# Optimization experiments

Hardware: AMD Instinct MI355X
Metric: run time of the kernel (lower is better)

Reference implementation:

```python
import jax, jax.numpy as jnp
import numpy as np

B, N, F, H, D, HID = 32, 256, 8, 8, 8, 512  # batch, stocks, features, heads, head_dim, hidden
NEG_SLOPE = 0.2
NEG_INF = -1e30


def setup_inputs() -> dict:
    key = jax.random.key(0)
    ks = jax.random.split(key, 20)
    feat = jax.random.normal(ks[0], (B, F, N), jnp.float32)
    adjs = [(jax.random.uniform(ks[1 + i], (B, N, N)) < 0.05).astype(jnp.float32) for i in range(3)]
    inputs = jnp.concatenate(adjs + [feat], axis=1)  # (B, 3N+F, N)
    s = 0.02  # xavier-ish gain used in the torch init
    stdv = 1.0 / np.sqrt(H * D)
    return {
        'inputs': inputs,
        'W_gat': jax.random.normal(ks[4], (3, HID, H * D), jnp.float32) * stdv,
        'Wu': jax.random.normal(ks[5], (3, H, D, 1), jnp.float32),
        'Wv': jax.random.normal(ks[6], (3, H, D, 1), jnp.float32),
        'b_gat': jax.random.normal(ks[7], (3, H * D), jnp.float32) * stdv,
        'projW': jax.random.normal(ks[8], (3, HID, H * D), jnp.float32) * s,
        'projB': jnp.zeros((3, H * D), jnp.float32),
        'w_self1': jax.random.normal(ks[9], (F, HID), jnp.float32) * s,
        'b_self1': jnp.zeros((HID,), jnp.float32),
        'w_mlp': jax.random.normal(ks[10], (3, H * D, HID), jnp.float32) * s,
        'b_mlp': jnp.zeros((3, HID), jnp.float32),
        'w_self2': jax.random.normal(ks[11], (HID, HID), jnp.float32) * s,
        'b_self2': jnp.zeros((HID,), jnp.float32),
        'sem_w1': jax.random.normal(ks[12], (HID, HID), jnp.float32) * s,
        'sem_b1': jnp.zeros((HID,), jnp.float32),
        'sem_w2': jax.random.normal(ks[13], (HID, 1), jnp.float32) * s,
        'gen_w': jax.random.normal(ks[14], (N * HID, N), jnp.float32) * s,
        'gen_b': jnp.zeros((N,), jnp.float32),
    }


def _mhgat(x, adj, W, Wu, Wv, b, pW, pB):
    # x: (B,N,HID), adj: (B,N,N)
    # rows of adj that are entirely zero are replaced by 1e-6 everywhere
    adj = jnp.where(jnp.all(adj == 0, axis=-1, keepdims=True), 1e-6, adj)
    sup = (x @ W).reshape(B, N, H, D).transpose(0, 2, 1, 3)  # (B,H,N,D)
    f1 = jnp.einsum('bhnd,hd->bhn', sup, Wu[..., 0])[:, :, None, :]  # (B,H,1,N)
    f2 = jnp.einsum('bhnd,hd->bhn', sup, Wv[..., 0])[:, :, :, None]  # (B,H,N,1)
    w = jax.nn.leaky_relu(f1 + f2, NEG_SLOPE)  # (B,H,N,N)
    mw = jnp.einsum('bhij,bjk->bhik', w, adj)  # matmul masking, as in torch source
    mask = mw != 0
    # torch.sparse.softmax: softmax over nonzero entries only, zeros elsewhere
    attn = jax.nn.softmax(jnp.where(mask, mw, NEG_INF), axis=3)
    attn = jnp.where(mask, attn, 0.0)
    out = (attn @ sup).transpose(0, 2, 1, 3).reshape(B, N, H * D) + b
    out = out + x @ pW + pB  # residual projection
    return jnp.tanh(out)


def reference(inputs, W_gat, Wu, Wv, b_gat, projW, projB, w_self1, b_self1,
              w_mlp, b_mlp, w_self2, b_self2, sem_w1, sem_b1, sem_w2, gen_w, gen_b):
    ind_adj = inputs[:, :N, :]
    pos_adj = inputs[:, N:2 * N, :]
    neg_adj = inputs[:, 2 * N:3 * N, :]
    x = inputs[:, 3 * N:, :].transpose(0, 2, 1)  # (B,N,F)
    support = x @ w_self1 + b_self1  # (B,N,HID)
    gat_out = [_mhgat(support, a, W_gat[i], Wu[i], Wv[i], b_gat[i], projW[i], projB[i])
               for i, a in enumerate([ind_adj, pos_adj, neg_adj])]
    ind_s, pos_s, neg_s = gat_out
    s2 = support @ w_self2 + b_self2
    ind_o = ind_s @ w_mlp[0] + b_mlp[0]
    pos_o = neg_s @ w_mlp[1] + b_mlp[1]  # NOTE: bug in original source preserved (uses neg_support)
    neg_o = neg_s @ w_mlp[2] + b_mlp[2]
    emb = jnp.stack([s2, ind_o, pos_o, neg_o], axis=1)  # (B,4,N,HID)
    # semantic fusion attention
    wsem = jnp.tanh(emb @ sem_w1 + sem_b1) @ sem_w2  # (B,4,N,1)
    beta = jax.nn.softmax(wsem, axis=1)
    fused = (beta * emb).sum(axis=1)  # (B,N,HID)
    # PairNorm PN-SI, scale=1
    xc = fused - fused.mean(axis=1, keepdims=True)
    xc = xc / jnp.sqrt(1e-6 + (xc ** 2).sum(axis=2, keepdims=True))
    # generator
    flat = xc.reshape(B, N * HID)
    return jax.nn.sigmoid(flat @ gen_w + gen_b)  # (B,N)
```

## Files before the change

kernel.cpp:

```cpp
#include <hip/hip_runtime.h>
#include <math.h>

#define Bk   32
#define Nk   256
#define Fk   8
#define Hk   8
#define Dk   8
#define HIDk 512
#define HDk  64
#define NROWk 776
#define CAPk 96

typedef __attribute__((ext_vector_type(8))) short short8;
typedef __attribute__((ext_vector_type(4))) float f32x4;

__device__ __forceinline__ float lrelu(float x){ return fmaxf(x, 0.2f*x); }

__device__ __forceinline__ unsigned short f2bf(float x){
  unsigned int u = __float_as_uint(x);
  unsigned int r = (u + 0x7fffu + ((u>>16)&1u)) >> 16;
  return (unsigned short)r;
}

__global__ void k_support(const float* __restrict__ inp, const float* __restrict__ w1,
                          const float* __restrict__ b1, float* __restrict__ support){
  int bn = blockIdx.x; int b = bn >> 8; int n = bn & 255;
  const float* xin = inp + (size_t)b*NROWk*Nk + (size_t)(3*Nk)*Nk + n;
  float x[8];
#pragma unroll
  for (int f=0; f<8; f++) x[f] = xin[(size_t)f*Nk];
  int t = threadIdx.x;
  for (int c = t; c < HIDk; c += 256){
    float s = b1[c];
#pragma unroll
    for (int f=0; f<8; f++) s += x[f]*w1[f*HIDk + c];
    support[(size_t)bn*HIDk + c] = s;
  }
}

__global__ void k_sup(const float* __restrict__ support, const float* __restrict__ W,
                      float* __restrict__ sup){
  __shared__ float srow[4][HIDk+1];
  int b = blockIdx.x >> 6; int n0 = (blockIdx.x & 63) << 2;
  int t = threadIdx.x;
  for (int i = t; i < 4*HIDk; i += 256)
    srow[i>>9][i&511] = support[((size_t)b*Nk + n0 + (i>>9))*HIDk + (i&511)];
  __syncthreads();
  int nl = t >> 6, hd = t & 63;
  const float* srw = srow[nl];
  float s = 0.f;
  for (int c=0;c<HIDk;c++) s += srw[c]*W[c*HDk + hd];
  int h = hd >> 3, d = hd & 7;
  sup[(((size_t)b*Hk + h)*Nk + (n0+nl))*Dk + d] = s;
}

__global__ void k_fuv(const float* __restrict__ sup, const float* __restrict__ Wu,
                      const float* __restrict__ Wv, float* __restrict__ fu, float* __restrict__ fv){
  int i = blockIdx.x*256 + threadIdx.x;
  int h = (i >> 8) & 7;
  const float* s = sup + (size_t)i*Dk;
  float a=0.f, v=0.f;
#pragma unroll
  for (int d=0; d<8; d++){ float sv = s[d]; a += sv*Wu[h*8+d]; v += sv*Wv[h*8+d]; }
  fu[i] = a; fv[i] = v;
}

__global__ void k_rowzero(const float* __restrict__ inp, int rowOff,
                          int* __restrict__ z_cnt, int* __restrict__ z_idx){
  int b = blockIdx.x >> 8, j = blockIdx.x & 255;
  float v = inp[(size_t)b*NROWk*Nk + (size_t)(rowOff+j)*Nk + threadIdx.x];
  __shared__ int flag;
  if (threadIdx.x==0) flag = 0;
  __syncthreads();
  if (v != 0.0f) atomicOr(&flag, 1);
  __syncthreads();
  if (threadIdx.x==0 && flag==0){ int idx = atomicAdd(&z_cnt[b], 1); z_idx[b*Nk + idx] = j; }
}

__global__ void k_csc(const float* __restrict__ inp, int rowOff,
                      int* __restrict__ col_cnt, int* __restrict__ row_idx){
  int b = blockIdx.x >> 8, k = blockIdx.x & 255;
  int j = threadIdx.x;
  __shared__ unsigned char nzf[Nk];
  nzf[j] = (inp[(size_t)b*NROWk*Nk + (size_t)(rowOff+j)*Nk + k] != 0.0f) ? 1 : 0;
  __syncthreads();
  if (j == 0){
    int c = 0; int base = (b*Nk + k)*CAPk;
    for (int jj=0; jj<Nk; jj++) if (nzf[jj]){ if (c < CAPk) row_idx[base + c] = jj; c++; }
    col_cnt[b*Nk + k] = (c > CAPk) ? CAPk : c;
  }
}

__global__ void k_zsum(const float* __restrict__ fu, const float* __restrict__ fv,
                       const int* __restrict__ z_cnt, const int* __restrict__ z_idx,
                       float* __restrict__ zsum){
  int i = blockIdx.x*256 + threadIdx.x;
  int bh = i >> 8; int b = bh >> 3;
  int zc = z_cnt[b];
  float fvi = fv[i], s = 0.f;
  for (int t=0; t<zc; t++){ float x = fvi + fu[(bh<<8) + z_idx[b*Nk+t]]; s += lrelu(x); }
  zsum[i] = s;
}

__global__ __launch_bounds__(256) void k_attn(const float* __restrict__ sup,
    const float* __restrict__ fu_g, const float* __restrict__ fv_g,
    const float* __restrict__ zsum_g, const int* __restrict__ z_cnt,
    const int* __restrict__ col_cnt, const int* __restrict__ row_idx,
    float* __restrict__ ao){
  __shared__ float fu_s[Nk];
  __shared__ float fvt[32];
  __shared__ float zs[32];
  __shared__ float sup_s[Nk*Dk];
  __shared__ float mw[32][Nk+1];
  __shared__ unsigned char maskk[Nk];
  int blk = blockIdx.x;
  int bh = blk >> 3;
  int b  = bh >> 3;
  int h  = bh & 7;
  int i0 = (blk & 7) << 5;
  int t = threadIdx.x;
  fu_s[t] = fu_g[(bh<<8) + t];
  if (t < 32){ fvt[t] = fv_g[(bh<<8) + i0 + t]; zs[t] = zsum_g[(bh<<8) + i0 + t]; }
  for (int i = t; i < Nk*Dk; i += 256) sup_s[i] = sup[(size_t)bh*Nk*Dk + i];
  int zc = z_cnt[b];
  int cnt = col_cnt[b*Nk + t];
  maskk[t] = (cnt > 0 || zc > 0) ? 1 : 0;
  __syncthreads();
  {
    float acc[32];
#pragma unroll
    for (int i=0;i<32;i++) acc[i]=0.f;
    const int* ridx = row_idx + (size_t)(b*Nk + t)*CAPk;
    for (int s=0;s<cnt;s++){
      float fuj = fu_s[ridx[s]];
#pragma unroll
      for (int i=0;i<32;i++){ float x = fvt[i] + fuj; acc[i] += fmaxf(x, 0.2f*x); }
    }
#pragma unroll
    for (int i=0;i<32;i++) mw[i][t] = acc[i] + 1e-6f*zs[i];
  }
  __syncthreads();
  int wv = t>>6, lane = t&63;
  for (int i = wv; i < 32; i += 4){
    float vals[4]; float m = -1e30f;
#pragma unroll
    for (int q=0;q<4;q++){ int kk = lane + (q<<6); float v = mw[i][kk]; vals[q]=v; if (maskk[kk]) m = fmaxf(m, v); }
#pragma unroll
    for (int s=32;s>0;s>>=1) m = fmaxf(m, __shfl_xor(m, s));
    float e[4]; float sum=0.f;
#pragma unroll
    for (int q=0;q<4;q++){ int kk = lane + (q<<6); float p = maskk[kk] ? expf(vals[q]-m) : 0.f; e[q]=p; sum+=p; }
#pragma unroll
    for (int s=32;s>0;s>>=1) sum += __shfl_xor(sum, s);
    float inv = (sum > 0.f) ? 1.f/sum : 0.f;
#pragma unroll
    for (int q=0;q<4;q++){ int kk = lane + (q<<6); mw[i][kk] = e[q]*inv; }
  }
  __syncthreads();
  int il = t>>3, d = t&7;
  float s = 0.f;
  for (int kk=0; kk<Nk; kk++) s += mw[il][kk]*sup_s[kk*Dk + d];
  ao[((size_t)b*Nk + i0 + il)*HDk + (h<<3) + d] = s;
}

__global__ void k_gatout(const float* __restrict__ ao, const float* __restrict__ support,
                         const float* __restrict__ pW, const float* __restrict__ pB,
                         const float* __restrict__ bg, float* __restrict__ gat){
  __shared__ float srow[4][HIDk+1];
  int b = blockIdx.x >> 6; int n0 = (blockIdx.x & 63) << 2;
  int t = threadIdx.x;
  for (int i = t; i < 4*HIDk; i += 256)
    srow[i>>9][i&511] = support[((size_t)b*Nk + n0 + (i>>9))*HIDk + (i&511)];
  __syncthreads();
  int nl = t >> 6, hd = t & 63;
  const float* srw = srow[nl];
  float s = pB[hd] + bg[hd];
  for (int c=0;c<HIDk;c++) s += srw[c]*pW[c*HDk + hd];
  size_t idx = ((size_t)b*Nk + n0 + nl)*HDk + hd;
  gat[idx] = tanhf(s + ao[idx]);
}

__global__ void k_prepT(const float* __restrict__ w_self2, const float* __restrict__ sem_w1,
                        unsigned short* __restrict__ w2T, unsigned short* __restrict__ w1T){
  __shared__ float tile[64][65];
  const float* src = blockIdx.y ? sem_w1 : w_self2;
  unsigned short* dst = blockIdx.y ? w1T : w2T;
  int tk = (blockIdx.x >> 3) << 6;
  int tn = (blockIdx.x & 7) << 6;
  int t = threadIdx.x;
  for (int i = t; i < 64*64; i += 256){
    int r = i >> 6, c = i & 63;
    tile[r][c] = src[(size_t)(tk + r)*HIDk + tn + c];
  }
  __syncthreads();
  for (int i = t; i < 64*64; i += 256){
    int r = i >> 6, c = i & 63;
    dst[(size_t)(tn + r)*HIDk + tk + c] = f2bf(tile[c][r]);
  }
}

template<int MODE, int NF>
__global__ __launch_bounds__(256) void k_gemm512(
    const float* __restrict__ A, const unsigned short* __restrict__ BT,
    const float* __restrict__ bias, const float* __restrict__ w2,
    float* __restrict__ outf){
  constexpr int NPB = NF*16;
  __shared__ uint4 As4[64*4];
  __shared__ uint4 Bs4[NPB*4];
  int row0 = blockIdx.x << 6;
  int col0 = blockIdx.y * NPB;
  int t = threadIdx.x;
  int w = t >> 6, l = t & 63;
  f32x4 acc[NF];
#pragma unroll
  for (int i=0;i<NF;i++) acc[i] = (f32x4){0.f,0.f,0.f,0.f};

  int lrA = t >> 2;
  int slot = t & 3;
  const float* aptr = A + (size_t)(row0 + lrA)*HIDk + slot*8;
  const unsigned short* bbase = BT + (size_t)col0*HIDk + slot*8;

  for (int kc = 0; kc < 512; kc += 32){
    float4 av0 = *(const float4*)(aptr + kc);
    float4 av1 = *(const float4*)(aptr + kc + 4);
    uint4 bv[NPB/64];
#pragma unroll
    for (int r = 0; r < NPB/64; r++){
      int ln = r*64 + lrA;
      bv[r] = *(const uint4*)(bbase + (size_t)ln*HIDk + kc);
    }
    uint4 apk;
    unsigned short* ap = (unsigned short*)&apk;
    ap[0]=f2bf(av0.x); ap[1]=f2bf(av0.y); ap[2]=f2bf(av0.z); ap[3]=f2bf(av0.w);
    ap[4]=f2bf(av1.x); ap[5]=f2bf(av1.y); ap[6]=f2bf(av1.z); ap[7]=f2bf(av1.w);
    __syncthreads();
    As4[(lrA<<2) + (slot ^ ((lrA>>1)&3))] = apk;
#pragma unroll
    for (int r = 0; r < NPB/64; r++){
      int ln = r*64 + lrA;
      Bs4[(ln<<2) + (slot ^ ((ln>>1)&3))] = bv[r];
    }
    __syncthreads();
    int aRow = (w<<4) + (l&15);
    int ks = l>>4;
    short8 af = *(const short8*)&As4[(aRow<<2) + (ks ^ ((aRow>>1)&3))];
#pragma unroll
    for (int nf = 0; nf < NF; nf++){
      int bRow = (nf<<4) + (l&15);
      short8 bfr = *(const short8*)&Bs4[(bRow<<2) + (ks ^ ((bRow>>1)&3))];
      acc[nf] = __builtin_amdgcn_mfma_f32_16x16x32_bf16(af, bfr, acc[nf], 0, 0, 0);
    }
  }
  int colB = l & 15, rg = l >> 4;
  if (MODE == 0){
#pragma unroll
    for (int nf = 0; nf < NF; nf++){
      int col = col0 + (nf<<4) + colB;
      float bb = bias[col];
#pragma unroll
      for (int r = 0; r < 4; r++){
        int m = row0 + (w<<4) + (rg<<2) + r;
        int mo = ((m>>8)<<10) + (m&255);
        outf[(size_t)mo*HIDk + col] = acc[nf][r] + bb;
      }
    }
  } else {
    float s0=0.f, s1=0.f, s2v=0.f, s3=0.f;
#pragma unroll
    for (int nf = 0; nf < NF; nf++){
      int col = col0 + (nf<<4) + colB;
      float bb = bias[col], wv = w2[col];
      s0  += tanhf(acc[nf][0]+bb)*wv;
      s1  += tanhf(acc[nf][1]+bb)*wv;
      s2v += tanhf(acc[nf][2]+bb)*wv;
      s3  += tanhf(acc[nf][3]+bb)*wv;
    }
#pragma unroll
    for (int mk = 1; mk < 16; mk <<= 1){
      s0  += __shfl_xor(s0, mk);  s1 += __shfl_xor(s1, mk);
      s2v += __shfl_xor(s2v, mk); s3 += __shfl_xor(s3, mk);
    }
    if (colB == 0){
      int m = row0 + (w<<4) + (rg<<2);
      outf[m+0]=s0; outf[m+1]=s1; outf[m+2]=s2v; outf[m+3]=s3;
    }
  }
}

__global__ void k_mlp(const float* __restrict__ gat, const float* __restrict__ W,
                      const float* __restrict__ bias, float* __restrict__ emb, int chan){
  __shared__ float g[8][HDk];
  int b = blockIdx.x >> 5; int n0 = (blockIdx.x & 31) << 3;
  int t = threadIdx.x;
  for (int i=t;i<8*HDk;i+=256) g[i>>6][i&63] = gat[((size_t)b*Nk + n0 + (i>>6))*HDk + (i&63)];
  __syncthreads();
  for (int pass=0;pass<2;pass++){
    int o = t + (pass<<8);
    float acc[8]={0,0,0,0,0,0,0,0};
    for (int c=0;c<HDk;c++){
      float wv = W[c*HIDk+o];
#pragma unroll
      for (int r=0;r<8;r++) acc[r] += g[r][c]*wv;
    }
    float bs = bias[o];
#pragma unroll
    for (int r=0;r<8;r++) emb[(((size_t)b*4 + chan)*Nk + n0+r)*HIDk + o] = acc[r]+bs;
  }
}

__global__ void k_fused(const float* __restrict__ emb, const float* __restrict__ wsem,
                        float* __restrict__ fused){
  int bn = blockIdx.x; int b = bn>>8, n = bn&255;
  float w0 = wsem[((b<<2)+0)*Nk+n], w1 = wsem[((b<<2)+1)*Nk+n];
  float w2 = wsem[((b<<2)+2)*Nk+n], w3 = wsem[((b<<2)+3)*Nk+n];
  float m = fmaxf(fmaxf(w0,w1),fmaxf(w2,w3));
  float e0=expf(w0-m),e1=expf(w1-m),e2=expf(w2-m),e3=expf(w3-m);
  float inv = 1.f/(e0+e1+e2+e3);
  e0*=inv; e1*=inv; e2*=inv; e3*=inv;
  const float* e = emb + (((size_t)(b<<2))*Nk + n)*HIDk;
  size_t cs = (size_t)Nk*HIDk;
  for (int o = threadIdx.x; o < HIDk; o += 128)
    fused[(size_t)bn*HIDk + o] = e0*e[o] + e1*e[o+cs] + e2*e[o+2*cs] + e3*e[o+3*cs];
}

__global__ void k_cmean(const float* __restrict__ fused, float* __restrict__ cmean){
  int b = blockIdx.x >> 1; int o = ((blockIdx.x & 1) << 8) + threadIdx.x;
  float s=0.f;
  for (int n=0;n<Nk;n++) s += fused[((size_t)b*Nk+n)*HIDk + o];
  cmean[b*HIDk+o] = s*(1.f/Nk);
}

__global__ void k_norm(const float* __restrict__ fused, const float* __restrict__ cmean,
                       float* __restrict__ xc){
  __shared__ float red[4];
  int bn = blockIdx.x; int b = bn>>8;
  int t = threadIdx.x;
  float v0 = fused[(size_t)bn*HIDk + t]       - cmean[b*HIDk + t];
  float v1 = fused[(size_t)bn*HIDk + t+256]   - cmean[b*HIDk + t+256];
  float ss = v0*v0 + v1*v1;
#pragma unroll
  for (int s=32;s>0;s>>=1) ss += __shfl_xor(ss, s);
  if ((t&63)==0) red[t>>6] = ss;
  __syncthreads();
  float tot = red[0]+red[1]+red[2]+red[3];
  float inv = 1.0f/sqrtf(1e-6f + tot);
  xc[(size_t)bn*HIDk + t]     = v0*inv;
  xc[(size_t)bn*HIDk + t+256] = v1*inv;
}

__global__ __launch_bounds__(256) void k_gen(const float* __restrict__ xc, const float* __restrict__ genw,
                                             float* __restrict__ part){
  __shared__ float xs[Bk*HIDk];
  int n = blockIdx.x; int t = threadIdx.x;
  for (int i=t; i<Bk*HIDk; i+=256) xs[i] = xc[((size_t)(i>>9)*Nk + n)*HIDk + (i&511)];
  __syncthreads();
  float acc[32];
#pragma unroll
  for (int b=0;b<32;b++) acc[b]=0.f;
  const float* wp = genw + (size_t)n*HIDk*Nk + t;
  for (int c=0;c<HIDk;c++){
    float wv = wp[(size_t)c*Nk];
#pragma unroll
    for (int b=0;b<32;b++) acc[b] += xs[(b<<9)+c]*wv;
  }
#pragma unroll
  for (int b=0;b<32;b++) part[((size_t)n*Bk + b)*Nk + t] = acc[b];
}

__global__ void k_final(const float* __restrict__ part, const float* __restrict__ genb,
                        float* __restrict__ out){
  int b = blockIdx.x, g = threadIdx.x;
  float s = genb[g];
  for (int n=0;n<Nk;n++) s += part[((size_t)n*Bk + b)*Nk + g];
  out[b*Nk + g] = 1.f/(1.f + expf(-s));
}

extern "C" void kernel_launch(void* const* d_in, const int* in_sizes, int n_in,
                              void* d_out, int out_size, void* d_ws, size_t ws_size,
                              hipStream_t stream){
  const float* inp    = (const float*)d_in[0];
  const float* W_gat  = (const float*)d_in[1];
  const float* Wu     = (const float*)d_in[2];
  const float* Wv     = (const float*)d_in[3];
  const float* b_gat  = (const float*)d_in[4];
  const float* projW  = (const float*)d_in[5];
  const float* projB  = (const float*)d_in[6];
  const float* w_self1= (const float*)d_in[7];
  const float* b_self1= (const float*)d_in[8];
  const float* w_mlp  = (const float*)d_in[9];
  const float* b_mlp  = (const float*)d_in[10];
  const float* w_self2= (const float*)d_in[11];
  const float* b_self2= (const float*)d_in[12];
  const float* sem_w1 = (const float*)d_in[13];
  const float* sem_b1 = (const float*)d_in[14];
  const float* sem_w2 = (const float*)d_in[15];
  const float* gen_w  = (const float*)d_in[16];
  const float* gen_b  = (const float*)d_in[17];
  float* out = (float*)d_out;
  (void)in_sizes; (void)n_in; (void)out_size; (void)ws_size;

  float* w = (float*)d_ws;
  size_t off = 0;
  auto A = [&](size_t n){ float* p = w + off; off += (n + 63) & ~(size_t)63; return p; };
  float* support = A((size_t)Bk*Nk*HIDk);
  float* emb     = A((size_t)Bk*4*Nk*HIDk);
  float* sup0 = A((size_t)Bk*Hk*Nk*Dk); float* sup1 = A((size_t)Bk*Hk*Nk*Dk);
  float* fu0  = A(Bk*Hk*Nk); float* fu1 = A(Bk*Hk*Nk);
  float* fv0  = A(Bk*Hk*Nk); float* fv1 = A(Bk*Hk*Nk);
  float* zs0  = A(Bk*Hk*Nk); float* zs1 = A(Bk*Hk*Nk);
  float* ao0  = A((size_t)Bk*Nk*HDk); float* ao1 = A((size_t)Bk*Nk*HDk);
  float* wsem = A(Bk*4*Nk);
  float* fused= A((size_t)Bk*Nk*HIDk);
  float* cmean= A(Bk*HIDk);
  float* part = A((size_t)Nk*Bk*Nk);
  float* tbuf = A(2*HIDk*HIDk/2);
  unsigned short* w2T = (unsigned short*)tbuf;
  unsigned short* w1T = w2T + HIDk*HIDk;
  int* ib  = (int*)(w + off);
  int* zc0 = ib;              int* zc1 = zc0 + Bk;
  int* zi0 = zc1 + Bk;        int* zi1 = zi0 + Bk*Nk;
  int* cc0 = zi1 + Bk*Nk;     int* cc1 = cc0 + Bk*Nk;
  int* ri0 = cc1 + Bk*Nk;     int* ri1 = ri0 + (size_t)Bk*Nk*CAPk;

  hipMemsetAsync(zc0, 0, 2*Bk*sizeof(int), stream);
  k_prepT<<<dim3(64,2), 256, 0, stream>>>(w_self2, sem_w1, w2T, w1T);
  k_support<<<Bk*Nk, 256, 0, stream>>>(inp, w_self1, b_self1, support);
  k_sup<<<Bk*(Nk/4), 256, 0, stream>>>(support, W_gat, sup0);
  k_sup<<<Bk*(Nk/4), 256, 0, stream>>>(support, W_gat + 2*HIDk*HDk, sup1);
  k_fuv<<<Bk*Hk*Nk/256, 256, 0, stream>>>(sup0, Wu, Wv, fu0, fv0);
  k_fuv<<<Bk*Hk*Nk/256, 256, 0, stream>>>(sup1, Wu + 2*Hk*Dk, Wv + 2*Hk*Dk, fu1, fv1);
  k_rowzero<<<Bk*Nk, 256, 0, stream>>>(inp, 0,    zc0, zi0);
  k_rowzero<<<Bk*Nk, 256, 0, stream>>>(inp, 2*Nk, zc1, zi1);
  k_csc<<<Bk*Nk, 256, 0, stream>>>(inp, 0,    cc0, ri0);
  k_csc<<<Bk*Nk, 256, 0, stream>>>(inp, 2*Nk, cc1, ri1);
  k_zsum<<<Bk*Hk*Nk/256, 256, 0, stream>>>(fu0, fv0, zc0, zi0, zs0);
  k_zsum<<<Bk*Hk*Nk/256, 256, 0, stream>>>(fu1, fv1, zc1, zi1, zs1);
  k_attn<<<Bk*Hk*(Nk/32), 256, 0, stream>>>(sup0, fu0, fv0, zs0, zc0, cc0, ri0, ao0);
  k_attn<<<Bk*Hk*(Nk/32), 256, 0, stream>>>(sup1, fu1, fv1, zs1, zc1, cc1, ri1, ao1);
  k_gatout<<<Bk*(Nk/4), 256, 0, stream>>>(ao0, support, projW,                projB,         b_gat,         ao0);
  k_gatout<<<Bk*(Nk/4), 256, 0, stream>>>(ao1, support, projW + 2*HIDk*HDk,   projB + 2*HDk, b_gat + 2*HDk, ao1);
  k_gemm512<0,16><<<dim3(128,2), 256, 0, stream>>>(support, w2T, b_self2, nullptr, emb);
  k_mlp<<<Bk*(Nk/8), 256, 0, stream>>>(ao0, w_mlp,               b_mlp,          emb, 1);
  k_mlp<<<Bk*(Nk/8), 256, 0, stream>>>(ao1, w_mlp + HDk*HIDk,    b_mlp + HIDk,   emb, 2);
  k_mlp<<<Bk*(Nk/8), 256, 0, stream>>>(ao1, w_mlp + 2*HDk*HIDk,  b_mlp + 2*HIDk, emb, 3);
  k_gemm512<1,32><<<dim3(512,1), 256, 0, stream>>>(emb, w1T, sem_b1, sem_w2, wsem);
  k_fused<<<Bk*Nk, 128, 0, stream>>>(emb, wsem, fused);
  k_cmean<<<Bk*2, 256, 0, stream>>>(fused, cmean);
  k_norm<<<Bk*Nk, 256, 0, stream>>>(fused, cmean, fused);
  k_gen<<<Nk, 256, 0, stream>>>(fused, gen_w, part);
  k_final<<<Bk, 256, 0, stream>>>(part, gen_b, out);
}
```

Measured before the change: 993.5 us.

## Narrow GEMM N-tile to 128, prefetch next K-chunk, split-N with atomic reduction

Both bf16 MFMA GEMMs now use a fixed 128-column tile, which multiplies the grid size (128x4 and 512x4 blocks) to raise occupancy and parallelism on the many CUs. Global loads for the next K chunk are issued after the shared-memory stores, so they overlap with the MFMA work on the current chunk. The semantic-attention GEMM splits its N dimension across 4 blocks and combines the partial tanh·w2 sums with float atomicAdd into a buffer that is zeroed first by an added memset. The cost is that the A tile is loaded four times as often, plus atomic traffic and non-deterministic summation order.

```diff
diff --git a/kernel.cpp b/kernel.cpp
--- a/kernel.cpp
+++ b/kernel.cpp
@@ -199,11 +199,12 @@
   }
 }
 
-template<int MODE, int NF>
+template<int MODE>
 __global__ __launch_bounds__(256) void k_gemm512(
     const float* __restrict__ A, const unsigned short* __restrict__ BT,
     const float* __restrict__ bias, const float* __restrict__ w2,
     float* __restrict__ outf){
+  constexpr int NF = 8;
   constexpr int NPB = NF*16;
   __shared__ uint4 As4[64*4];
   __shared__ uint4 Bs4[NPB*4];
@@ -218,29 +219,32 @@
   int lrA = t >> 2;
   int slot = t & 3;
   const float* aptr = A + (size_t)(row0 + lrA)*HIDk + slot*8;
-  const unsigned short* bbase = BT + (size_t)col0*HIDk + slot*8;
+  const unsigned short* bbase = BT + (size_t)(col0 + lrA)*HIDk + slot*8;
+
+  float4 av0 = *(const float4*)(aptr);
+  float4 av1 = *(const float4*)(aptr + 4);
+  uint4 bv0  = *(const uint4*)(bbase);
+  uint4 bv1  = *(const uint4*)(bbase + (size_t)64*HIDk);
 
   for (int kc = 0; kc < 512; kc += 32){
-    float4 av0 = *(const float4*)(aptr + kc);
-    float4 av1 = *(const float4*)(aptr + kc + 4);
-    uint4 bv[NPB/64];
-#pragma unroll
-    for (int r = 0; r < NPB/64; r++){
-      int ln = r*64 + lrA;
-      bv[r] = *(const uint4*)(bbase + (size_t)ln*HIDk + kc);
-    }
     uint4 apk;
     unsigned short* ap = (unsigned short*)&apk;
     ap[0]=f2bf(av0.x); ap[1]=f2bf(av0.y); ap[2]=f2bf(av0.z); ap[3]=f2bf(av0.w);
     ap[4]=f2bf(av1.x); ap[5]=f2bf(av1.y); ap[6]=f2bf(av1.z); ap[7]=f2bf(av1.w);
     __syncthreads();
     As4[(lrA<<2) + (slot ^ ((lrA>>1)&3))] = apk;
-#pragma unroll
-    for (int r = 0; r < NPB/64; r++){
-      int ln = r*64 + lrA;
-      Bs4[(ln<<2) + (slot ^ ((ln>>1)&3))] = bv[r];
+    Bs4[(lrA<<2) + (slot ^ ((lrA>>1)&3))] = bv0;
+    {
+      int ln = 64 + lrA;
+      Bs4[(ln<<2) + (slot ^ ((ln>>1)&3))] = bv1;
     }
     __syncthreads();
+    if (kc + 32 < 512){
+      av0 = *(const float4*)(aptr + kc + 32);
+      av1 = *(const float4*)(aptr + kc + 36);
+      bv0 = *(const uint4*)(bbase + kc + 32);
+      bv1 = *(const uint4*)(bbase + (size_t)64*HIDk + kc + 32);
+    }
     int aRow = (w<<4) + (l&15);
     int ks = l>>4;
     short8 af = *(const short8*)&As4[(aRow<<2) + (ks ^ ((aRow>>1)&3))];
@@ -282,7 +286,10 @@
     }
     if (colB == 0){
       int m = row0 + (w<<4) + (rg<<2);
-      outf[m+0]=s0; outf[m+1]=s1; outf[m+2]=s2v; outf[m+3]=s3;
+      atomicAdd(&outf[m+0], s0);
+      atomicAdd(&outf[m+1], s1);
+      atomicAdd(&outf[m+2], s2v);
+      atomicAdd(&outf[m+3], s3);
     }
   }
 }
@@ -423,6 +430,7 @@
   int* ri0 = cc1 + Bk*Nk;     int* ri1 = ri0 + (size_t)Bk*Nk*CAPk;
 
   hipMemsetAsync(zc0, 0, 2*Bk*sizeof(int), stream);
+  hipMemsetAsync(wsem, 0, (size_t)Bk*4*Nk*sizeof(float), stream);
   k_prepT<<<dim3(64,2), 256, 0, stream>>>(w_self2, sem_w1, w2T, w1T);
   k_support<<<Bk*Nk, 256, 0, stream>>>(inp, w_self1, b_self1, support);
   k_sup<<<Bk*(Nk/4), 256, 0, stream>>>(support, W_gat, sup0);
@@ -439,11 +447,11 @@
   k_attn<<<Bk*Hk*(Nk/32), 256, 0, stream>>>(sup1, fu1, fv1, zs1, zc1, cc1, ri1, ao1);
   k_gatout<<<Bk*(Nk/4), 256, 0, stream>>>(ao0, support, projW,                projB,         b_gat,         ao0);
   k_gatout<<<Bk*(Nk/4), 256, 0, stream>>>(ao1, support, projW + 2*HIDk*HDk,   projB + 2*HDk, b_gat + 2*HDk, ao1);
-  k_gemm512<0,16><<<dim3(128,2), 256, 0, stream>>>(support, w2T, b_self2, nullptr, emb);
+  k_gemm512<0><<<dim3(128,4), 256, 0, stream>>>(support, w2T, b_self2, nullptr, emb);
   k_mlp<<<Bk*(Nk/8), 256, 0, stream>>>(ao0, w_mlp,               b_mlp,          emb, 1);
   k_mlp<<<Bk*(Nk/8), 256, 0, stream>>>(ao1, w_mlp + HDk*HIDk,    b_mlp + HIDk,   emb, 2);
   k_mlp<<<Bk*(Nk/8), 256, 0, stream>>>(ao1, w_mlp + 2*HDk*HIDk,  b_mlp + 2*HIDk, emb, 3);
-  k_gemm512<1,32><<<dim3(512,1), 256, 0, stream>>>(emb, w1T, sem_b1, sem_w2, wsem);
+  k_gemm512<1><<<dim3(512,4), 256, 0, stream>>>(emb, w1T, sem_b1, sem_w2, wsem);
   k_fused<<<Bk*Nk, 128, 0, stream>>>(emb, wsem, fused);
   k_cmean<<<Bk*2, 256, 0, stream>>>(fused, cmean);
   k_norm<<<Bk*Nk, 256, 0, stream>>>(fused, cmean, fused);
```

New measurement: 891.9 us. 1.11x faster.
